# Kernel optimization log

Hardware: AMD Instinct MI355X
Metric: run time of the kernel (lower is better)

## Reference

```python
import jax, jax.numpy as jnp
import numpy as np

TEMPERATURE = 0.07
BASE_TEMPERATURE = 0.07


def setup_inputs() -> dict:
    key = jax.random.key(0)
    k1, k2 = jax.random.split(key)
    features = jax.random.normal(k1, (4096, 2, 128), dtype=jnp.float32)
    labels = jax.random.randint(k2, (4096,), 0, 100, dtype=jnp.int64)
    return {"features": features, "labels": labels}


def reference(features, labels):
    # features: [B, n_views, D], labels: [B]
    B, n_views, D = features.shape
    N = B * n_views

    # label equality mask [B, B]
    lab = labels.reshape(-1, 1)
    mask = (lab == lab.T).astype(jnp.float32)

    # flatten views (C-order, same as torch .view) and L2-normalize
    feat = features.reshape(N, D)
    feat = feat / jnp.clip(jnp.linalg.norm(feat, axis=1, keepdims=True), 1e-12)

    # similarity logits [N, N]
    logits = jnp.matmul(feat, feat.T) / TEMPERATURE
    logits_max = jax.lax.stop_gradient(jnp.max(logits, axis=1, keepdims=True))
    logits = logits - logits_max

    # tile mask to [N, N] (torch .repeat ordering) and remove self-contrast
    mask = jnp.tile(mask, (n_views, n_views))
    logits_mask = 1.0 - jnp.eye(N, dtype=jnp.float32)
    mask = mask * logits_mask

    exp_logits = jnp.exp(logits) * logits_mask
    log_prob = logits - jnp.log(jnp.sum(exp_logits, axis=1, keepdims=True) + 1e-12)

    mask_pos_pairs = jnp.clip(jnp.sum(mask, axis=1), 1.0)
    mean_log_prob_pos = jnp.sum(mask * log_prob, axis=1) / mask_pos_pairs

    loss = -(TEMPERATURE / BASE_TEMPERATURE) * mean_log_prob_pos
    return jnp.mean(loss.reshape(n_views, B))
```

## Files before the change

kernel.cpp:

```cpp
#include <hip/hip_runtime.h>
#include <hip/hip_bf16.h>
#include <hip/hip_fp8.h>
#include <math.h>

#define NB 4096
#define NN 8192
#define DD 128
#define NCLS 100
#define NSPLIT 16
#define CHUNK 64
#define NCHUNK 8

constexpr float INV_T = 14.285714285714286f;
constexpr float EC1   = 20.609929155556620f;
constexpr float EC0   = -20.609929155556620f;
constexpr float LN2   = 0.6931471805599453f;

typedef unsigned char u8;
typedef __attribute__((ext_vector_type(8))) int   v8i;
typedef __attribute__((ext_vector_type(4))) int   v4i;
typedef __attribute__((ext_vector_type(4))) float f32x4;

__global__ __launch_bounds__(256) void k_norm(const float* __restrict__ feat,
                                              u8* __restrict__ fb8,
                                              float* __restrict__ selfdot,
                                              float* __restrict__ out) {
    const int gid = blockIdx.x * 256 + threadIdx.x;
    if (gid == 0) out[0] = 0.0f;
    const int r    = gid >> 6;
    const int lane = threadIdx.x & 63;
    const float2 v = ((const float2*)(feat + (size_t)r * DD))[lane];
    float ss = v.x * v.x + v.y * v.y;
#pragma unroll
    for (int off = 1; off < 64; off <<= 1) ss += __shfl_xor(ss, off, 64);
    const float scale = 1.0f / fmaxf(sqrtf(ss), 1e-12f);
    const __hip_fp8_e4m3 qx(v.x * scale), qy(v.y * scale);
    const unsigned short pack = (unsigned short)qx.__x |
                                ((unsigned short)qy.__x << 8);
    ((unsigned short*)(fb8 + (size_t)r * DD))[lane] = pack;
    const float xb = (float)qx, yb = (float)qy;
    float s2 = xb * xb + yb * yb;
#pragma unroll
    for (int off = 1; off < 64; off <<= 1) s2 += __shfl_xor(s2, off, 64);
    if (lane == 0) selfdot[r] = s2;
}

__device__ __forceinline__ void stage_chunk(const u8* __restrict__ fb8, u8* sbuf,
                                            int jb, int w, int n15, int q) {
#pragma unroll
    for (int h = 0; h < 2; ++h) {
        const int p = w * 2 + h;
        const u8* g = fb8 + (size_t)(jb + (p >> 1) * 16 + n15) * DD + q * 32 + (p & 1) * 16;
        __builtin_amdgcn_global_load_lds(
            (const __attribute__((address_space(1))) void*)g,
            (__attribute__((address_space(3))) void*)(sbuf + p * 1024),
            16, 0, 0);
    }
}

__global__ __launch_bounds__(256, 4) void k_main(const u8* __restrict__ fb8,
                                                 const int* __restrict__ labels,
                                                 float* __restrict__ g_se,
                                                 float* __restrict__ g_ps) {
    __shared__ u8 sB[2][CHUNK * DD];
    __shared__ int slab[512];

    const int tid  = threadIdx.x;
    const int lane = tid & 63;
    const int w    = tid >> 6;
    const int rb   = blockIdx.x >> 4;
    const int js   = blockIdx.x & (NSPLIT - 1);
    const int i0   = rb * 128 + w * 32;
    const int jb0  = js * 512;
    const int q    = lane >> 4;
    const int n15  = lane & 15;

    slab[tid]       = labels[(jb0 + tid) & (NB - 1)];
    slab[tid + 256] = labels[(jb0 + tid + 256) & (NB - 1)];

    v8i af[2];
#pragma unroll
    for (int tt = 0; tt < 2; ++tt) {
        const u8* rp = fb8 + (size_t)(i0 + tt * 16 + n15) * DD + q * 32;
        const v4i lo = *(const v4i*)rp;
        const v4i hi = *(const v4i*)(rp + 16);
        v8i a;
#pragma unroll
        for (int k = 0; k < 4; ++k) { a[k] = lo[k]; a[4 + k] = hi[k]; }
        af[tt] = a;
    }
    int labi[8];
#pragma unroll
    for (int tt = 0; tt < 2; ++tt)
#pragma unroll
        for (int r = 0; r < 4; ++r)
            labi[tt * 4 + r] = labels[(i0 + tt * 16 + q * 4 + r) & (NB - 1)];

    float a_se[8] = {}, a_ps[8] = {};

    stage_chunk(fb8, &sB[0][0], jb0, w, n15, q);
    __syncthreads();

    for (int c = 0; c < NCHUNK; ++c) {
        if (c + 1 < NCHUNK)
            stage_chunk(fb8, &sB[(c + 1) & 1][0], jb0 + (c + 1) * CHUNK, w, n15, q);
        const u8* sb = &sB[c & 1][0];
        const int crel = c * CHUNK;
#pragma unroll
        for (int jt = 0; jt < 4; ++jt) {
            const v4i lo = *(const v4i*)(sb + (jt * 2 + 0) * 1024 + lane * 16);
            const v4i hi = *(const v4i*)(sb + (jt * 2 + 1) * 1024 + lane * 16);
            v8i bb;
#pragma unroll
            for (int k = 0; k < 4; ++k) { bb[k] = lo[k]; bb[4 + k] = hi[k]; }
            const int labj = slab[crel + jt * 16 + n15];
            f32x4 a0 = {0.f, 0.f, 0.f, 0.f}, a1 = {0.f, 0.f, 0.f, 0.f};
            a0 = __builtin_amdgcn_mfma_scale_f32_16x16x128_f8f6f4(
                     af[0], bb, a0, 0, 0, 0, 0x7F7F7F7F, 0, 0x7F7F7F7F);
            a1 = __builtin_amdgcn_mfma_scale_f32_16x16x128_f8f6f4(
                     af[1], bb, a1, 0, 0, 0, 0x7F7F7F7F, 0, 0x7F7F7F7F);
#pragma unroll
            for (int r = 0; r < 4; ++r) {
                const float d0 = a0[r], d1 = a1[r];
                a_se[r]     += __builtin_amdgcn_exp2f(fmaf(d0, EC1, EC0));
                a_se[4 + r] += __builtin_amdgcn_exp2f(fmaf(d1, EC1, EC0));
                a_ps[r]     += (labi[r]     == labj) ? d0 : 0.0f;
                a_ps[4 + r] += (labi[4 + r] == labj) ? d1 : 0.0f;
            }
        }
        __syncthreads();
    }

#pragma unroll
    for (int s = 0; s < 8; ++s) {
        float v1 = a_se[s], v2 = a_ps[s];
#pragma unroll
        for (int off = 1; off < 16; off <<= 1) {
            v1 += __shfl_xor(v1, off, 64);
            v2 += __shfl_xor(v2, off, 64);
        }
        if (n15 == 0) {
            const int row = i0 + (s >> 2) * 16 + q * 4 + (s & 3);
            g_se[js * NN + row] = v1;
            g_ps[js * NN + row] = v2;
        }
    }
}

__global__ __launch_bounds__(256) void k_final(const int* __restrict__ labels,
                                               const float* __restrict__ g_se,
                                               const float* __restrict__ g_ps,
                                               const float* __restrict__ selfdot,
                                               float* __restrict__ out) {
    __shared__ int hist[NCLS];
    const int tid = threadIdx.x;
    for (int i = tid; i < NCLS; i += 256) hist[i] = 0;
    __syncthreads();
    for (int b = tid; b < NB; b += 256) atomicAdd(&hist[labels[b]], 1);
    __syncthreads();

    const int r = blockIdx.x * 256 + tid;
    const int c = labels[r & (NB - 1)];
    float se = 0.f, ps = 0.f;
#pragma unroll
    for (int t = 0; t < NSPLIT; ++t) {
        se += g_se[t * NN + r];
        ps += g_ps[t * NN + r];
    }
    const float sd = selfdot[r];
    se -= __builtin_amdgcn_exp2f(fmaf(sd, EC1, EC0));
    const float ct = (float)(2 * hist[c] - 1);
    const float possum = INV_T * ((ps - sd) - ct);
    const float lg  = __builtin_amdgcn_logf(se + 1e-12f) * LN2;
    const float mlpp = (possum - ct * lg) / fmaxf(ct, 1.0f);
    float v = -mlpp * (1.0f / (float)NN);
#pragma unroll
    for (int off = 1; off < 64; off <<= 1) v += __shfl_xor(v, off, 64);
    __shared__ float sred[4];
    if ((tid & 63) == 0) sred[tid >> 6] = v;
    __syncthreads();
    if (tid == 0) atomicAdd(out, sred[0] + sred[1] + sred[2] + sred[3]);
}

extern "C" void kernel_launch(void* const* d_in, const int* in_sizes, int n_in,
                              void* d_out, int out_size, void* d_ws, size_t ws_size,
                              hipStream_t stream) {
    const float* feat = (const float*)d_in[0];
    const int* labels = (const int*)d_in[1];
    float* out        = (float*)d_out;
    char* ws          = (char*)d_ws;

    u8* fb8         = (u8*)ws;
    float* g_se     = (float*)(ws + (size_t)1 * 1024 * 1024);
    float* g_ps     = g_se + NSPLIT * NN;
    float* selfdot  = g_ps + NSPLIT * NN;

    k_norm<<<NN / 4, 256, 0, stream>>>(feat, fb8, selfdot, out);
    k_main<<<(NN / 128) * NSPLIT, 256, 0, stream>>>(fb8, labels, g_se, g_ps);
    k_final<<<NN / 256, 256, 0, stream>>>(labels, g_se, g_ps, selfdot, out);
}
```

Before: 82.97 us.

## Replace per-pair positive masking with per-class feature sums and prescale features

```diff
diff --git a/kernel.cpp b/kernel.cpp
--- a/kernel.cpp
+++ b/kernel.cpp
@@ -8,11 +8,12 @@
 #define DD 128
 #define NCLS 100
 #define NSPLIT 16
-#define CHUNK 64
-#define NCHUNK 8
+#define CHUNK 128
+#define NCHUNK 4
 
 constexpr float INV_T = 14.285714285714286f;
 constexpr float EC1   = 20.609929155556620f;
+constexpr float SQE   = 4.5398160926378074f;
 constexpr float EC0   = -20.609929155556620f;
 constexpr float LN2   = 0.6931471805599453f;
 
@@ -20,6 +21,10 @@
 typedef __attribute__((ext_vector_type(8))) int   v8i;
 typedef __attribute__((ext_vector_type(4))) int   v4i;
 typedef __attribute__((ext_vector_type(4))) float f32x4;
+
+__device__ __forceinline__ float fp8tof(u8 b) {
+    __hip_fp8_e4m3 t; t.__x = b; return (float)t;
+}
 
 __global__ __launch_bounds__(256) void k_norm(const float* __restrict__ feat,
                                               u8* __restrict__ fb8,
@@ -33,7 +38,7 @@
     float ss = v.x * v.x + v.y * v.y;
 #pragma unroll
     for (int off = 1; off < 64; off <<= 1) ss += __shfl_xor(ss, off, 64);
-    const float scale = 1.0f / fmaxf(sqrtf(ss), 1e-12f);
+    const float scale = SQE / fmaxf(sqrtf(ss), 1e-12f);
     const __hip_fp8_e4m3 qx(v.x * scale), qy(v.y * scale);
     const unsigned short pack = (unsigned short)qx.__x |
                                 ((unsigned short)qy.__x << 8);
@@ -48,8 +53,8 @@
 __device__ __forceinline__ void stage_chunk(const u8* __restrict__ fb8, u8* sbuf,
                                             int jb, int w, int n15, int q) {
 #pragma unroll
-    for (int h = 0; h < 2; ++h) {
-        const int p = w * 2 + h;
+    for (int h = 0; h < 4; ++h) {
+        const int p = w * 4 + h;
         const u8* g = fb8 + (size_t)(jb + (p >> 1) * 16 + n15) * DD + q * 32 + (p & 1) * 16;
         __builtin_amdgcn_global_load_lds(
             (const __attribute__((address_space(1))) void*)g,
@@ -61,9 +66,9 @@
 __global__ __launch_bounds__(256, 4) void k_main(const u8* __restrict__ fb8,
                                                  const int* __restrict__ labels,
                                                  float* __restrict__ g_se,
-                                                 float* __restrict__ g_ps) {
+                                                 float* __restrict__ S,
+                                                 int* __restrict__ counts) {
     __shared__ u8 sB[2][CHUNK * DD];
-    __shared__ int slab[512];
 
     const int tid  = threadIdx.x;
     const int lane = tid & 63;
@@ -75,9 +80,6 @@
     const int q    = lane >> 4;
     const int n15  = lane & 15;
 
-    slab[tid]       = labels[(jb0 + tid) & (NB - 1)];
-    slab[tid + 256] = labels[(jb0 + tid + 256) & (NB - 1)];
-
     v8i af[2];
 #pragma unroll
     for (int tt = 0; tt < 2; ++tt) {
@@ -89,14 +91,8 @@
         for (int k = 0; k < 4; ++k) { a[k] = lo[k]; a[4 + k] = hi[k]; }
         af[tt] = a;
     }
-    int labi[8];
-#pragma unroll
-    for (int tt = 0; tt < 2; ++tt)
-#pragma unroll
-        for (int r = 0; r < 4; ++r)
-            labi[tt * 4 + r] = labels[(i0 + tt * 16 + q * 4 + r) & (NB - 1)];
-
-    float a_se[8] = {}, a_ps[8] = {};
+
+    float a_se[8] = {};
 
     stage_chunk(fb8, &sB[0][0], jb0, w, n15, q);
     __syncthreads();
@@ -105,15 +101,13 @@
         if (c + 1 < NCHUNK)
             stage_chunk(fb8, &sB[(c + 1) & 1][0], jb0 + (c + 1) * CHUNK, w, n15, q);
         const u8* sb = &sB[c & 1][0];
-        const int crel = c * CHUNK;
-#pragma unroll
-        for (int jt = 0; jt < 4; ++jt) {
+#pragma unroll
+        for (int jt = 0; jt < 8; ++jt) {
             const v4i lo = *(const v4i*)(sb + (jt * 2 + 0) * 1024 + lane * 16);
             const v4i hi = *(const v4i*)(sb + (jt * 2 + 1) * 1024 + lane * 16);
             v8i bb;
 #pragma unroll
             for (int k = 0; k < 4; ++k) { bb[k] = lo[k]; bb[4 + k] = hi[k]; }
-            const int labj = slab[crel + jt * 16 + n15];
             f32x4 a0 = {0.f, 0.f, 0.f, 0.f}, a1 = {0.f, 0.f, 0.f, 0.f};
             a0 = __builtin_amdgcn_mfma_scale_f32_16x16x128_f8f6f4(
                      af[0], bb, a0, 0, 0, 0, 0x7F7F7F7F, 0, 0x7F7F7F7F);
@@ -121,11 +115,8 @@
                      af[1], bb, a1, 0, 0, 0, 0x7F7F7F7F, 0, 0x7F7F7F7F);
 #pragma unroll
             for (int r = 0; r < 4; ++r) {
-                const float d0 = a0[r], d1 = a1[r];
-                a_se[r]     += __builtin_amdgcn_exp2f(fmaf(d0, EC1, EC0));
-                a_se[4 + r] += __builtin_amdgcn_exp2f(fmaf(d1, EC1, EC0));
-                a_ps[r]     += (labi[r]     == labj) ? d0 : 0.0f;
-                a_ps[4 + r] += (labi[4 + r] == labj) ? d1 : 0.0f;
+                a_se[r]     += __builtin_amdgcn_exp2f(a0[r]);
+                a_se[4 + r] += __builtin_amdgcn_exp2f(a1[r]);
             }
         }
         __syncthreads();
@@ -133,53 +124,82 @@
 
 #pragma unroll
     for (int s = 0; s < 8; ++s) {
-        float v1 = a_se[s], v2 = a_ps[s];
-#pragma unroll
-        for (int off = 1; off < 16; off <<= 1) {
-            v1 += __shfl_xor(v1, off, 64);
-            v2 += __shfl_xor(v2, off, 64);
+        float v = a_se[s];
+#pragma unroll
+        for (int off = 1; off < 16; off <<= 1) v += __shfl_xor(v, off, 64);
+        if (n15 == 0)
+            g_se[js * NN + i0 + (s >> 2) * 16 + q * 4 + (s & 3)] = v;
+    }
+
+    if (blockIdx.x >= 1024 - NCLS) {
+        const int c = blockIdx.x - (1024 - NCLS);
+        __syncthreads();
+        int* list = (int*)&sB[0][0];
+        __shared__ int lcnt;
+        if (tid == 0) lcnt = 0;
+        __syncthreads();
+        for (int b = tid; b < NB; b += 256)
+            if (labels[b] == c) list[atomicAdd(&lcnt, 1)] = b;
+        __syncthreads();
+        const int cnt = lcnt;
+        const int d = tid & 127;
+        const int h = tid >> 7;
+        float acc0 = 0.0f, acc1 = 0.0f;
+        int i = 0;
+        for (; i + 1 < cnt; i += 2) {
+            const int b0 = list[i], b1 = list[i + 1];
+            acc0 += fp8tof(fb8[(size_t)(b0 + h * NB) * DD + d]);
+            acc1 += fp8tof(fb8[(size_t)(b1 + h * NB) * DD + d]);
         }
-        if (n15 == 0) {
-            const int row = i0 + (s >> 2) * 16 + q * 4 + (s & 3);
-            g_se[js * NN + row] = v1;
-            g_ps[js * NN + row] = v2;
-        }
-    }
-}
-
-__global__ __launch_bounds__(256) void k_final(const int* __restrict__ labels,
+        if (i < cnt) acc0 += fp8tof(fb8[(size_t)(list[i] + h * NB) * DD + d]);
+        __syncthreads();
+        float* Sl = (float*)&sB[0][0];
+        Sl[tid] = acc0 + acc1;
+        __syncthreads();
+        if (tid < 128) S[c * DD + tid] = Sl[tid] + Sl[tid + 128];
+        if (tid == 0) counts[c] = cnt;
+    }
+}
+
+__global__ __launch_bounds__(256) void k_final(const u8* __restrict__ fb8,
+                                               const int* __restrict__ labels,
                                                const float* __restrict__ g_se,
-                                               const float* __restrict__ g_ps,
+                                               const float* __restrict__ S,
+                                               const int* __restrict__ counts,
                                                const float* __restrict__ selfdot,
                                                float* __restrict__ out) {
-    __shared__ int hist[NCLS];
-    const int tid = threadIdx.x;
-    for (int i = tid; i < NCLS; i += 256) hist[i] = 0;
-    __syncthreads();
-    for (int b = tid; b < NB; b += 256) atomicAdd(&hist[labels[b]], 1);
-    __syncthreads();
-
-    const int r = blockIdx.x * 256 + tid;
+    const int r = blockIdx.x * 256 + threadIdx.x;
     const int c = labels[r & (NB - 1)];
-    float se = 0.f, ps = 0.f;
-#pragma unroll
-    for (int t = 0; t < NSPLIT; ++t) {
-        se += g_se[t * NN + r];
-        ps += g_ps[t * NN + r];
+    float se = 0.0f;
+#pragma unroll
+    for (int t = 0; t < NSPLIT; ++t) se += g_se[t * NN + r];
+
+    const u8* fp = fb8 + (size_t)r * DD;
+    const float* sp = S + c * DD;
+    float s1 = 0.0f;
+#pragma unroll
+    for (int k = 0; k < DD; k += 4) {
+        const unsigned int u = *(const unsigned int*)(fp + k);
+        const float4 sv = *(const float4*)(sp + k);
+        s1 = fmaf(fp8tof(u & 0xff), sv.x,
+             fmaf(fp8tof((u >> 8) & 0xff), sv.y,
+             fmaf(fp8tof((u >> 16) & 0xff), sv.z,
+             fmaf(fp8tof(u >> 24), sv.w, s1))));
     }
     const float sd = selfdot[r];
-    se -= __builtin_amdgcn_exp2f(fmaf(sd, EC1, EC0));
-    const float ct = (float)(2 * hist[c] - 1);
-    const float possum = INV_T * ((ps - sd) - ct);
+    const float C0 = __builtin_amdgcn_exp2f(EC0);
+    se = (se - __builtin_amdgcn_exp2f(sd)) * C0;
+    const float ct = (float)(2 * counts[c] - 1);
+    const float possum = INV_T * ((s1 - sd) * (1.0f / EC1) - ct);
     const float lg  = __builtin_amdgcn_logf(se + 1e-12f) * LN2;
     const float mlpp = (possum - ct * lg) / fmaxf(ct, 1.0f);
     float v = -mlpp * (1.0f / (float)NN);
 #pragma unroll
     for (int off = 1; off < 64; off <<= 1) v += __shfl_xor(v, off, 64);
     __shared__ float sred[4];
-    if ((tid & 63) == 0) sred[tid >> 6] = v;
+    if ((threadIdx.x & 63) == 0) sred[threadIdx.x >> 6] = v;
     __syncthreads();
-    if (tid == 0) atomicAdd(out, sred[0] + sred[1] + sred[2] + sred[3]);
+    if (threadIdx.x == 0) atomicAdd(out, sred[0] + sred[1] + sred[2] + sred[3]);
 }
 
 extern "C" void kernel_launch(void* const* d_in, const int* in_sizes, int n_in,
@@ -192,10 +212,11 @@
 
     u8* fb8         = (u8*)ws;
     float* g_se     = (float*)(ws + (size_t)1 * 1024 * 1024);
-    float* g_ps     = g_se + NSPLIT * NN;
-    float* selfdot  = g_ps + NSPLIT * NN;
+    float* selfdot  = g_se + NSPLIT * NN;
+    float* S        = selfdot + NN;
+    int*   counts   = (int*)(S + NCLS * DD);
 
     k_norm<<<NN / 4, 256, 0, stream>>>(feat, fb8, selfdot, out);
-    k_main<<<(NN / 128) * NSPLIT, 256, 0, stream>>>(fb8, labels, g_se, g_ps);
-    k_final<<<NN / 256, 256, 0, stream>>>(labels, g_se, g_ps, selfdot, out);
-}
+    k_main<<<(NN / 128) * NSPLIT, 256, 0, stream>>>(fb8, labels, g_se, S, counts);
+    k_final<<<NN / 256, 256, 0, stream>>>(fb8, labels, g_se, S, counts, selfdot, out);
+}
```

Result: slower. 268.3 us (+223.4%).
